# Optimization experiments

Measured on AMD Instinct MI355X. Metric: run time of the kernel, lower is better.

Reference implementation:

```python
import jax, jax.numpy as jnp
import numpy as np

H = 4096        # hidden_size
NH = 32         # num_attention_heads
NKV = 8         # num_key_value_heads
HD = H // NH    # head_dim = 128
N_REP = NH // NKV
SCALE = HD ** -0.5


def _rope(x, cos, sin):
    # x: (B, h, S, HD); cos/sin: (S, HD//2) broadcast over batch/heads
    x1 = x[..., 0::2]
    x2 = x[..., 1::2]
    return jnp.concatenate([x1 * cos - x2 * sin, x1 * sin + x2 * cos], axis=-1)


def setup_inputs() -> dict:
    key = jax.random.key(0)
    ks = jax.random.split(key, 9)
    B, S = 2, 2048
    return {
        "hidden_states": jax.random.normal(ks[0], (B, S, H), jnp.float32),
        "cos": jax.random.uniform(ks[1], (S, HD // 2), jnp.float32),
        "sin": jax.random.uniform(ks[2], (S, HD // 2), jnp.float32),
        "Wq": jax.random.normal(ks[3], (H, H), jnp.float32) * (H ** -0.5),
        "Wk": jax.random.normal(ks[4], (NKV * HD, H), jnp.float32) * (H ** -0.5),
        "bk": jax.random.normal(ks[5], (NKV * HD,), jnp.float32) * 0.01,
        "Wv": jax.random.normal(ks[6], (NKV * HD, H), jnp.float32) * (H ** -0.5),
        "bv": jax.random.normal(ks[7], (NKV * HD,), jnp.float32) * 0.01,
        "Wo": jax.random.normal(ks[8], (H, H), jnp.float32) * (H ** -0.5),
    }


def reference(hidden_states, cos, sin, Wq, Wk, bk, Wv, bv, Wo):
    B, S, _ = hidden_states.shape
    # projections (torch Linear: x @ W.T + b)
    q = (hidden_states @ Wq.T).reshape(B, S, NH, HD).transpose(0, 2, 1, 3)
    k = (hidden_states @ Wk.T + bk).reshape(B, S, NKV, HD).transpose(0, 2, 1, 3)
    v = (hidden_states @ Wv.T + bv).reshape(B, S, NKV, HD).transpose(0, 2, 1, 3)
    q = _rope(q, cos, sin)
    k = _rope(k, cos, sin)
    # GQA repeat_kv: (B, NKV, S, HD) -> (B, NH, S, HD)
    k = jnp.repeat(k, N_REP, axis=1)
    v = jnp.repeat(v, N_REP, axis=1)
    # full attention (no mask is actually applied in the source forward)
    scores = jnp.einsum('bhqd,bhkd->bhqk', q, k) * SCALE
    attn = jax.nn.softmax(scores, axis=-1)
    out = jnp.einsum('bhqk,bhkd->bhqd', attn, v)
    out = out.transpose(0, 2, 1, 3).reshape(B, S, H)
    return out @ Wo.T
```

## Files before the change

kernel.cpp:

```cpp
#include <hip/hip_runtime.h>

typedef unsigned short u16;
typedef short short8 __attribute__((ext_vector_type(8)));
typedef float floatx4 __attribute__((ext_vector_type(4)));

#define H_ 4096
#define NH_ 32
#define NKV_ 8
#define HD_ 128
#define SEQ_ 2048
#define BATCH_ 2
#define ROWS_ (BATCH_*SEQ_)
#define KVW_ (NKV_*HD_)
#define NQKV_ (H_ + 2*KVW_)
#define VSTRIDE_ NQKV_
#define SCALE_ 0.08838834764831845f
#define TSCALE_ (SCALE_*1.442695040888963f)

__device__ __forceinline__ u16 f2bf(float f) {
  union { float f; unsigned u; } x; x.f = f;
  unsigned r = x.u + 0x7fffu + ((x.u >> 16) & 1u);
  return (u16)(r >> 16);
}
__device__ __forceinline__ float bf2f(u16 h) {
  union { unsigned u; float f; } x; x.u = ((unsigned)h) << 16;
  return x.f;
}
__device__ __forceinline__ unsigned cvt_pk_bf16(float lo, float hi) {
  unsigned r;
  asm("v_cvt_pk_bf16_f32 %0, %1, %2" : "=v"(r) : "v"(lo), "v"(hi));
  return r;
}

__global__ __launch_bounds__(256) void cvt_f32_bf16(const float* __restrict__ src,
                                                    u16* __restrict__ dst, int n4) {
  int i = blockIdx.x * 256 + threadIdx.x;
  if (i >= n4) return;
  float4 v = ((const float4*)src)[i];
  ushort4 o;
  o.x = f2bf(v.x); o.y = f2bf(v.y); o.z = f2bf(v.z); o.w = f2bf(v.w);
  ((ushort4*)dst)[i] = o;
}

__global__ __launch_bounds__(256) void bias_concat(const float* __restrict__ bk,
                                                   const float* __restrict__ bv,
                                                   float* __restrict__ dst) {
  int i = blockIdx.x * 256 + threadIdx.x;
  if (i >= NQKV_) return;
  float v = 0.f;
  if (i >= H_ + KVW_)      v = bv[i - (H_ + KVW_)];
  else if (i >= H_)        v = bk[i - H_];
  dst[i] = v;
}

template<int BF16_OUT, int HAS_BIAS>
__global__ __launch_bounds__(512, 2) void gemm_nt_8p(const u16* __restrict__ A, const u16* __restrict__ B,
                                                     const float* __restrict__ bias, void* __restrict__ Cout,
                                                     int M, int N, int K)
{
  __shared__ __align__(16) u16 lds[65536];
  char* ldsB = (char*)lds;
  const int tid  = threadIdx.x;
  const int lane = tid & 63;
  const int wave = tid >> 6;
  const int ln   = lane & 15;
  const int quad = lane >> 4;
  const int wm   = wave >> 2;
  const int wn   = wave & 3;

  const int NB  = N >> 8;
  const int nwg = gridDim.x;
  const int cpx = nwg >> 3;
  const int l   = (blockIdx.x & 7) * cpx + (blockIdx.x >> 3);
  const int m0  = (l / NB) * 256;
  const int n0  = (l % NB) * 256;

  const u16* srcp[4][2];
  {
    int ob0 = wave*2048 + lane*16;
#pragma unroll
    for (int h = 0; h < 4; ++h) {
#pragma unroll
      for (int j = 0; j < 2; ++j) {
        int ob  = ob0 + j*1024;
        int row = ob >> 6;
        int sl  = ((ob >> 4) & 3) ^ ((row >> 1) & 3);
        int kst = h >> 1;
        if ((h & 1) == 0) srcp[h][j] = A + (size_t)(m0 + row)*K + kst*32 + sl*8;
        else              srcp[h][j] = B + (size_t)(n0 + row)*K + kst*32 + sl*8;
      }
    }
  }

#define STAGE(h_, p_, kt_)                                                          \
  {                                                                                 \
    __builtin_amdgcn_global_load_lds(                                               \
      (const __attribute__((address_space(1))) void*)(srcp[h_][0] + (kt_)*64),      \
      (__attribute__((address_space(3))) void*)(ldsB + (((h_)&1)*65536 + (p_)*32768 \
          + ((h_)>>1)*16384 + wave*2048)), 16, 0, 0);                               \
    __builtin_amdgcn_global_load_lds(                                               \
      (const __attribute__((address_space(1))) void*)(srcp[h_][1] + (kt_)*64),      \
      (__attribute__((address_space(3))) void*)(ldsB + (((h_)&1)*65536 + (p_)*32768 \
          + ((h_)>>1)*16384 + wave*2048 + 1024)), 16, 0, 0);                        \
  }

  const int slq16 = (quad ^ ((ln >> 1) & 3)) * 16;
  const int aoffL = (wm*128 + ln)*64 + slq16;
  const int boffL = (wn*64  + ln)*64 + slq16;

  floatx4 zf = {0.f, 0.f, 0.f, 0.f};
  floatx4 acc[8][4];
#pragma unroll
  for (int i = 0; i < 8; ++i)
#pragma unroll
    for (int j = 0; j < 4; ++j) acc[i][j] = zf;

  STAGE(0, 0, 0) STAGE(1, 0, 0) STAGE(2, 0, 0) STAGE(3, 0, 0)
  asm volatile("s_waitcnt vmcnt(4)");
  __builtin_amdgcn_s_barrier();

  const int NT = K >> 6;
  for (int t = 0; t < NT; ++t) {
    const int p  = t & 1;
    const int np = p ^ 1;
    const char* ab = ldsB + p*32768;
    const char* bb = ldsB + 65536 + p*32768;
    short8 af[4], bq[4];

#pragma unroll
    for (int j = 0; j < 4; ++j) bq[j] = *(const short8*)(bb + boffL + j*1024);
#pragma unroll
    for (int i = 0; i < 4; ++i) af[i] = *(const short8*)(ab + aoffL + i*1024);
    if (t + 1 < NT) STAGE(0, np, t+1)
    __builtin_amdgcn_s_barrier();
    asm volatile("s_waitcnt lgkmcnt(0)");
    __builtin_amdgcn_sched_barrier(0);
    __builtin_amdgcn_s_setprio(1);
#pragma unroll
    for (int i = 0; i < 4; ++i)
#pragma unroll
      for (int j = 0; j < 4; ++j)
        acc[i][j] = __builtin_amdgcn_mfma_f32_16x16x32_bf16(af[i], bq[j], acc[i][j], 0, 0, 0);
    __builtin_amdgcn_s_setprio(0);
    __builtin_amdgcn_s_barrier();

#pragma unroll
    for (int i = 0; i < 4; ++i) af[i] = *(const short8*)(ab + aoffL + (4+i)*1024);
    if (t + 1 < NT) STAGE(1, np, t+1)
    __builtin_amdgcn_s_barrier();
    asm volatile("s_waitcnt lgkmcnt(0)");
    __builtin_amdgcn_sched_barrier(0);
    __builtin_amdgcn_s_setprio(1);
#pragma unroll
    for (int i = 0; i < 4; ++i)
#pragma unroll
      for (int j = 0; j < 4; ++j)
        acc[4+i][j] = __builtin_amdgcn_mfma_f32_16x16x32_bf16(af[i], bq[j], acc[4+i][j], 0, 0, 0);
    __builtin_amdgcn_s_setprio(0);
    if (t + 1 < NT) { asm volatile("s_waitcnt vmcnt(4)"); }
    else            { asm volatile("s_waitcnt vmcnt(0)"); }
    __builtin_amdgcn_s_barrier();

#pragma unroll
    for (int j = 0; j < 4; ++j) bq[j] = *(const short8*)(bb + 16384 + boffL + j*1024);
#pragma unroll
    for (int i = 0; i < 4; ++i) af[i] = *(const short8*)(ab + 16384 + aoffL + i*1024);
    if (t + 1 < NT) STAGE(2, np, t+1)
    __builtin_amdgcn_s_barrier();
    asm volatile("s_waitcnt lgkmcnt(0)");
    __builtin_amdgcn_sched_barrier(0);
    __builtin_amdgcn_s_setprio(1);
#pragma unroll
    for (int i = 0; i < 4; ++i)
#pragma unroll
      for (int j = 0; j < 4; ++j)
        acc[i][j] = __builtin_amdgcn_mfma_f32_16x16x32_bf16(af[i], bq[j], acc[i][j], 0, 0, 0);
    __builtin_amdgcn_s_setprio(0);
    __builtin_amdgcn_s_barrier();

#pragma unroll
    for (int i = 0; i < 4; ++i) af[i] = *(const short8*)(ab + 16384 + aoffL + (4+i)*1024);
    if (t + 1 < NT) STAGE(3, np, t+1)
    __builtin_amdgcn_s_barrier();
    asm volatile("s_waitcnt lgkmcnt(0)");
    __builtin_amdgcn_sched_barrier(0);
    __builtin_amdgcn_s_setprio(1);
#pragma unroll
    for (int i = 0; i < 4; ++i)
#pragma unroll
      for (int j = 0; j < 4; ++j)
        acc[4+i][j] = __builtin_amdgcn_mfma_f32_16x16x32_bf16(af[i], bq[j], acc[4+i][j], 0, 0, 0);
    __builtin_amdgcn_s_setprio(0);
    if (t + 1 < NT) { asm volatile("s_waitcnt vmcnt(4)"); }
    __builtin_amdgcn_s_barrier();
  }
#undef STAGE

#pragma unroll
  for (int i = 0; i < 8; ++i) {
#pragma unroll
    for (int j = 0; j < 4; ++j) {
      int row = m0 + wm*128 + i*16 + quad*4;
      int col = n0 + wn*64  + j*16 + ln;
      float bv_ = HAS_BIAS ? bias[col] : 0.f;
#pragma unroll
      for (int r = 0; r < 4; ++r) {
        float v = acc[i][j][r] + bv_;
        if (BF16_OUT) ((u16*)Cout)[(size_t)(row+r)*N + col] = f2bf(v);
        else          ((float*)Cout)[(size_t)(row+r)*N + col] = v;
      }
    }
  }
}

template<int BF16_OUT, int HAS_BIAS>
__global__ __launch_bounds__(512, 2) void gemm_nt_8p_h(const u16* __restrict__ A, const u16* __restrict__ B,
                                                       const float* __restrict__ bias, void* __restrict__ Cout,
                                                       int M, int N, int K)
{
  __shared__ __align__(16) u16 lds[49152];
  char* ldsB = (char*)lds;
  const int tid  = threadIdx.x;
  const int lane = tid & 63;
  const int wave = tid >> 6;
  const int ln   = lane & 15;
  const int quad = lane >> 4;
  const int wm   = wave >> 2;
  const int wn   = wave & 3;

  const int NB  = N >> 8;
  const int nwg = gridDim.x;
  const int cpx = nwg >> 3;
  const int l   = (blockIdx.x & 7) * cpx + (blockIdx.x >> 3);
  const int m0  = (l / NB) * 128;
  const int n0  = (l % NB) * 256;

  const u16* srcA[2];
  const u16* srcB[2][2];
  {
    int ob  = wave*1024 + lane*16;
    int row = ob >> 6;
    int sl  = ((ob >> 4) & 3) ^ ((row >> 1) & 3);
#pragma unroll
    for (int kst = 0; kst < 2; ++kst)
      srcA[kst] = A + (size_t)(m0 + row)*K + kst*32 + sl*8;
  }
#pragma unroll
  for (int j = 0; j < 2; ++j) {
    int ob  = wave*2048 + j*1024 + lane*16;
    int row = ob >> 6;
    int sl  = ((ob >> 4) & 3) ^ ((row >> 1) & 3);
#pragma unroll
    for (int kst = 0; kst < 2; ++kst)
      srcB[kst][j] = B + (size_t)(n0 + row)*K + kst*32 + sl*8;
  }

#define STAGEH(kst_, p_, kt_)                                                        \
  {                                                                                  \
    __builtin_amdgcn_global_load_lds(                                                \
      (const __attribute__((address_space(1))) void*)(srcA[kst_] + (kt_)*64),        \
      (__attribute__((address_space(3))) void*)(ldsB + ((p_)*16384 + (kst_)*8192     \
          + wave*1024)), 16, 0, 0);                                                  \
    __builtin_amdgcn_global_load_lds(                                                \
      (const __attribute__((address_space(1))) void*)(srcB[kst_][0] + (kt_)*64),     \
      (__attribute__((address_space(3))) void*)(ldsB + (32768 + (p_)*32768           \
          + (kst_)*16384 + wave*2048)), 16, 0, 0);                                   \
    __builtin_amdgcn_global_load_lds(                                                \
      (const __attribute__((address_space(1))) void*)(srcB[kst_][1] + (kt_)*64),     \
      (__attribute__((address_space(3))) void*)(ldsB + (32768 + (p_)*32768           \
          + (kst_)*16384 + wave*2048 + 1024)), 16, 0, 0);                            \
  }

  const int slq16 = (quad ^ ((ln >> 1) & 3)) * 16;
  const int aoffL = (wm*64 + ln)*64 + slq16;
  const int boffL = (wn*64 + ln)*64 + slq16;

  floatx4 zf = {0.f, 0.f, 0.f, 0.f};
  floatx4 acc[4][4];
#pragma unroll
  for (int i = 0; i < 4; ++i)
#pragma unroll
    for (int j = 0; j < 4; ++j) acc[i][j] = zf;

  STAGEH(0, 0, 0) STAGEH(1, 0, 0)
  asm volatile("s_waitcnt vmcnt(3)");
  __builtin_amdgcn_s_barrier();

  const int NT = K >> 6;
  for (int t = 0; t < NT; ++t) {
    const int p  = t & 1;
    const int np = p ^ 1;
    const char* ab = ldsB + p*16384;
    const char* bb = ldsB + 32768 + p*32768;
    short8 af[4], bq[4];

#pragma unroll
    for (int j = 0; j < 4; ++j) bq[j] = *(const short8*)(bb + boffL + j*1024);
#pragma unroll
    for (int i = 0; i < 4; ++i) af[i] = *(const short8*)(ab + aoffL + i*1024);
    if (t + 1 < NT) STAGEH(0, np, t+1)
    __builtin_amdgcn_s_barrier();
    asm volatile("s_waitcnt lgkmcnt(0)");
    __builtin_amdgcn_sched_barrier(0);
    __builtin_amdgcn_s_setprio(1);
#pragma unroll
    for (int i = 0; i < 4; ++i)
#pragma unroll
      for (int j = 0; j < 4; ++j)
        acc[i][j] = __builtin_amdgcn_mfma_f32_16x16x32_bf16(af[i], bq[j], acc[i][j], 0, 0, 0);
    __builtin_amdgcn_s_setprio(0);
    if (t + 1 < NT) { asm volatile("s_waitcnt vmcnt(3)"); }
    else            { asm volatile("s_waitcnt vmcnt(0)"); }
    __builtin_amdgcn_s_barrier();

#pragma unroll
    for (int j = 0; j < 4; ++j) bq[j] = *(const short8*)(bb + 16384 + boffL + j*1024);
#pragma unroll
    for (int i = 0; i < 4; ++i) af[i] = *(const short8*)(ab + 8192 + aoffL + i*1024);
    if (t + 1 < NT) STAGEH(1, np, t+1)
    __builtin_amdgcn_s_barrier();
    asm volatile("s_waitcnt lgkmcnt(0)");
    __builtin_amdgcn_sched_barrier(0);
    __builtin_amdgcn_s_setprio(1);
#pragma unroll
    for (int i = 0; i < 4; ++i)
#pragma unroll
      for (int j = 0; j < 4; ++j)
        acc[i][j] = __builtin_amdgcn_mfma_f32_16x16x32_bf16(af[i], bq[j], acc[i][j], 0, 0, 0);
    __builtin_amdgcn_s_setprio(0);
    if (t + 1 < NT) { asm volatile("s_waitcnt vmcnt(3)"); }
    __builtin_amdgcn_s_barrier();
  }
#undef STAGEH

#pragma unroll
  for (int i = 0; i < 4; ++i) {
#pragma unroll
    for (int j = 0; j < 4; ++j) {
      int row = m0 + wm*64 + i*16 + quad*4;
      int col = n0 + wn*64 + j*16 + ln;
      float bv_ = HAS_BIAS ? bias[col] : 0.f;
#pragma unroll
      for (int r = 0; r < 4; ++r) {
        float v = acc[i][j][r] + bv_;
        if (BF16_OUT) ((u16*)Cout)[(size_t)(row+r)*N + col] = f2bf(v);
        else          ((float*)Cout)[(size_t)(row+r)*N + col] = v;
      }
    }
  }
}

__global__ __launch_bounds__(256) void rope_kernel(const u16* __restrict__ X, u16* __restrict__ Y,
                                                   const float* __restrict__ cosb, const float* __restrict__ sinb,
                                                   int nheads, int total, int istride, int ostride)
{
  int idx = blockIdx.x * 256 + threadIdx.x;
  if (idx >= total) return;
  int d = idx & 63;
  int t = idx >> 6;
  int hh = t % nheads;
  int row = t / nheads;
  int s = row & (SEQ_ - 1);
  size_t bi = (size_t)row * istride + hh * HD_;
  size_t bo = (size_t)row * ostride + hh * HD_;
  float x1 = bf2f(X[bi + 2*d]);
  float x2 = bf2f(X[bi + 2*d + 1]);
  float c  = cosb[s*64 + d];
  float sn = sinb[s*64 + d];
  Y[bo + d]      = f2bf(x1*c - x2*sn);
  Y[bo + 64 + d] = f2bf(x1*sn + x2*c);
}

#define KS_TILE (64*128)

__global__ __launch_bounds__(512, 2) void attn_fwd(const u16* __restrict__ Q, const u16* __restrict__ K,
                                                   const u16* __restrict__ V, u16* __restrict__ O)
{
  __shared__ __align__(16) u16 Ks[2*KS_TILE];
  __shared__ __align__(16) u16 Vt[128*72];
  const int tid  = threadIdx.x;
  const int lane = tid & 63;
  const int wave = tid >> 6;
  const int ln   = lane & 15;
  const int quad = lane >> 4;
  const int lin = (blockIdx.x & 7) * 64 + (blockIdx.x >> 3);
  const int bh  = lin >> 3;
  const int b   = bh >> 5;
  const int h   = bh & 31;
  const int kvh = h >> 2;
  const int q0  = (lin & 7) * 256;

  short8 qf[2][4];
#pragma unroll
  for (int mt = 0; mt < 2; ++mt) {
    const u16* qbase = Q + (size_t)(b*SEQ_ + q0 + wave*32 + mt*16 + ln) * H_ + h * HD_;
#pragma unroll
    for (int kst = 0; kst < 4; ++kst)
      qf[mt][kst] = *(const short8*)(qbase + kst*32 + quad*8);
  }

  short8 bones;
  {
    short v1 = (ln == 0) ? (short)0x3F80 : (short)0;
#pragma unroll
    for (int j = 0; j < 8; ++j) bones[j] = v1;
  }

  int kou[2];
  const u16* ks0[2];
#pragma unroll
  for (int i = 0; i < 2; ++i) {
    int ou = wave*2048 + i*1024;
    int ob = ou + lane*16;
    int key = ob >> 8;
    int dgp = (ob >> 4) & 15;
    int dgl = dgp ^ (key & 15);
    kou[i] = ou;
    ks0[i] = K + (size_t)(b*SEQ_ + key)*KVW_ + kvh*HD_ + dgl*8;
  }
  const int g  = tid & 15;
  const int dg = (tid >> 4) & 15;
  const int j2 = tid >> 8;
  const u16* vs0 = V + (size_t)(b*SEQ_ + j2*32 + g)*VSTRIDE_ + kvh*HD_ + dg*8;
  const int k0v = ((g >> 1) & 1)*32 + (g >> 2)*8 + (g & 1)*4 + j2*2;

  floatx4 zf = {0.f, 0.f, 0.f, 0.f};
  floatx4 o[2][8];
  floatx4 ol[2];
#pragma unroll
  for (int mt = 0; mt < 2; ++mt) {
    ol[mt] = zf;
#pragma unroll
    for (int jt = 0; jt < 8; ++jt) o[mt][jt] = zf;
  }
  float mrow[2] = {-1e30f, -1e30f};

  int4 vreg[2];
#pragma unroll
  for (int i = 0; i < 2; ++i)
    __builtin_amdgcn_global_load_lds((const __attribute__((address_space(1))) void*)ks0[i],
        (__attribute__((address_space(3))) void*)((char*)Ks + kou[i]), 16, 0, 0);
#pragma unroll
  for (int jj = 0; jj < 2; ++jj)
    vreg[jj] = *(const int4*)(vs0 + (size_t)(jj*16)*VSTRIDE_);
  {
    union { int4 v; u16 u[8]; } w[2];
    w[0].v = vreg[0]; w[1].v = vreg[1];
#pragma unroll
    for (int dd = 0; dd < 8; ++dd) {
      ushort2 t2; t2.x = w[0].u[dd]; t2.y = w[1].u[dd];
      *(ushort2*)&Vt[(dg*8 + dd)*72 + k0v] = t2;
    }
  }
  __syncthreads();

  const int NT = SEQ_ / 64;
  for (int t = 0; t < NT; ++t) {
    if (t + 1 < NT) {
      size_t roff = (size_t)(t+1) * 64 * KVW_;
      char* kb = (char*)Ks + ((t+1)&1) * (KS_TILE*2);
#pragma unroll
      for (int i = 0; i < 2; ++i)
        __builtin_amdgcn_global_load_lds((const __attribute__((address_space(1))) void*)(ks0[i] + roff),
            (__attribute__((address_space(3))) void*)(kb + kou[i]), 16, 0, 0);
      size_t voff = (size_t)(t+1) * 64 * VSTRIDE_;
#pragma unroll
      for (int jj = 0; jj < 2; ++jj)
        vreg[jj] = *(const int4*)(vs0 + voff + (size_t)(jj*16)*VSTRIDE_);
    }
    const u16* Kc = Ks + (t&1)*KS_TILE;

    floatx4 s[2][4];
#pragma unroll
    for (int nt = 0; nt < 4; ++nt) { s[0][nt] = zf; s[1][nt] = zf; }
    __builtin_amdgcn_s_setprio(1);
#pragma unroll
    for (int kst = 0; kst < 4; ++kst) {
      int dgp = (kst*4 + quad) ^ ln;
#pragma unroll
      for (int nt = 0; nt < 4; ++nt) {
        short8 kf = *(const short8*)&Kc[(nt*16 + ln)*128 + dgp*8];
        s[0][nt] = __builtin_amdgcn_mfma_f32_16x16x32_bf16(kf, qf[0][kst], s[0][nt], 0, 0, 0);
        s[1][nt] = __builtin_amdgcn_mfma_f32_16x16x32_bf16(kf, qf[1][kst], s[1][nt], 0, 0, 0);
      }
    }
    __builtin_amdgcn_s_setprio(0);

    float rmv[2];
    bool ok = true;
#pragma unroll
    for (int mt = 0; mt < 2; ++mt) {
      float m0_ = fmaxf(fmaxf(s[mt][0][0], s[mt][0][1]), fmaxf(s[mt][0][2], s[mt][0][3]));
      float m1_ = fmaxf(fmaxf(s[mt][1][0], s[mt][1][1]), fmaxf(s[mt][1][2], s[mt][1][3]));
      float m2_ = fmaxf(fmaxf(s[mt][2][0], s[mt][2][1]), fmaxf(s[mt][2][2], s[mt][2][3]));
      float m3_ = fmaxf(fmaxf(s[mt][3][0], s[mt][3][1]), fmaxf(s[mt][3][2], s[mt][3][3]));
      float rm = fmaxf(fmaxf(m0_, m1_), fmaxf(m2_, m3_)) * TSCALE_;
      rm = fmaxf(rm, __shfl_xor(rm, 16));
      rm = fmaxf(rm, __shfl_xor(rm, 32));
      rmv[mt] = rm;
      ok = ok && (rm - mrow[mt] <= 8.0f);
    }
    if (!__all(ok)) {
#pragma unroll
      for (int mt = 0; mt < 2; ++mt) {
        float mn = fmaxf(mrow[mt], rmv[mt]);
        float al = exp2f(mrow[mt] - mn);
        mrow[mt] = mn;
        float av[4];
#pragma unroll
        for (int r = 0; r < 4; ++r) av[r] = __shfl(al, (lane & 48) | (quad*4 + r));
#pragma unroll
        for (int r = 0; r < 4; ++r) {
          float a_ = av[r];
#pragma unroll
          for (int jt = 0; jt < 8; ++jt) o[mt][jt][r] *= a_;
          ol[mt][r] *= a_;
        }
      }
    }
    short8 pa[2][2];
#pragma unroll
    for (int mt = 0; mt < 2; ++mt) {
      float mn = mrow[mt];
      float p[4][4];
#pragma unroll
      for (int nt = 0; nt < 4; ++nt)
#pragma unroll
        for (int r = 0; r < 4; ++r)
          p[r][nt] = exp2f(fmaf(s[mt][nt][r], TSCALE_, -mn));
#pragma unroll
      for (int k2 = 0; k2 < 2; ++k2) {
        union { unsigned u[4]; short8 v; } pk;
        pk.u[0] = cvt_pk_bf16(p[2*k2][0],   p[2*k2][1]);
        pk.u[1] = cvt_pk_bf16(p[2*k2][2],   p[2*k2][3]);
        pk.u[2] = cvt_pk_bf16(p[2*k2+1][0], p[2*k2+1][1]);
        pk.u[3] = cvt_pk_bf16(p[2*k2+1][2], p[2*k2+1][3]);
        pa[mt][k2] = pk.v;
      }
    }

    __builtin_amdgcn_s_setprio(1);
#pragma unroll
    for (int k2 = 0; k2 < 2; ++k2) {
#pragma unroll
      for (int jt = 0; jt < 8; ++jt) {
        short8 vf = *(const short8*)&Vt[(jt*16 + ln)*72 + k2*32 + quad*8];
        o[0][jt] = __builtin_amdgcn_mfma_f32_16x16x32_bf16(pa[0][k2], vf, o[0][jt], 0, 0, 0);
        o[1][jt] = __builtin_amdgcn_mfma_f32_16x16x32_bf16(pa[1][k2], vf, o[1][jt], 0, 0, 0);
      }
      ol[0] = __builtin_amdgcn_mfma_f32_16x16x32_bf16(pa[0][k2], bones, ol[0], 0, 0, 0);
      ol[1] = __builtin_amdgcn_mfma_f32_16x16x32_bf16(pa[1][k2], bones, ol[1], 0, 0, 0);
    }
    __builtin_amdgcn_s_setprio(0);

    __syncthreads();
    if (t + 1 < NT) {
      union { int4 v; u16 u[8]; } w[2];
      w[0].v = vreg[0]; w[1].v = vreg[1];
#pragma unroll
      for (int dd = 0; dd < 8; ++dd) {
        ushort2 t2; t2.x = w[0].u[dd]; t2.y = w[1].u[dd];
        *(ushort2*)&Vt[(dg*8 + dd)*72 + k0v] = t2;
      }
    }
    __syncthreads();
  }

#pragma unroll
  for (int mt = 0; mt < 2; ++mt) {
#pragma unroll
    for (int r = 0; r < 4; ++r) {
      float lv = __shfl(ol[mt][r], lane & 48);
      float inv = 1.f / lv;
      size_t row = (size_t)(b*SEQ_ + q0 + wave*32 + mt*16 + quad*4 + r);
      u16* dst = O + row * H_ + h * HD_ + ln;
#pragma unroll
      for (int jt = 0; jt < 8; ++jt)
        dst[jt*16] = f2bf(o[mt][jt][r] * inv);
    }
  }
}

extern "C" void kernel_launch(void* const* d_in, const int* in_sizes, int n_in,
                              void* d_out, int out_size, void* d_ws, size_t ws_size,
                              hipStream_t stream) {
  const float* hs   = (const float*)d_in[0];
  const float* cosb = (const float*)d_in[1];
  const float* sinb = (const float*)d_in[2];
  const float* Wq   = (const float*)d_in[3];
  const float* Wk   = (const float*)d_in[4];
  const float* bk   = (const float*)d_in[5];
  const float* Wv   = (const float*)d_in[6];
  const float* bv   = (const float*)d_in[7];
  const float* Wo   = (const float*)d_in[8];
  float* out = (float*)d_out;

  char* ws = (char*)d_ws;
  u16*   hs_bf   = (u16*)(ws +          0);
  u16*   Wqkv_bf = (u16*)(ws +   33554432);
  u16*   Wo_bf   = (u16*)(ws +   83886080);
  u16*   QKV0    = (u16*)(ws +  117440512);
  u16*   Qr      = (u16*)(ws +  167772160);
  u16*   Kr      = (u16*)(ws +  201326592);
  float* biasqkv = (float*)(ws + 209715200);
  u16*   Oa      = hs_bf;

  {
    int n;
    n = ROWS_*H_;  cvt_f32_bf16<<<(n/4 + 255)/256, 256, 0, stream>>>(hs, hs_bf, n/4);
    n = H_*H_;     cvt_f32_bf16<<<(n/4 + 255)/256, 256, 0, stream>>>(Wq, Wqkv_bf, n/4);
    n = KVW_*H_;   cvt_f32_bf16<<<(n/4 + 255)/256, 256, 0, stream>>>(Wk, Wqkv_bf + (size_t)H_*H_, n/4);
    n = KVW_*H_;   cvt_f32_bf16<<<(n/4 + 255)/256, 256, 0, stream>>>(Wv, Wqkv_bf + (size_t)(H_+KVW_)*H_, n/4);
    n = H_*H_;     cvt_f32_bf16<<<(n/4 + 255)/256, 256, 0, stream>>>(Wo, Wo_bf, n/4);
    bias_concat<<<(NQKV_ + 255)/256, 256, 0, stream>>>(bk, bv, biasqkv);
  }

  gemm_nt_8p_h<1,1><<<dim3((ROWS_/128)*(NQKV_/256)), dim3(512), 0, stream>>>(hs_bf, Wqkv_bf, biasqkv, QKV0, ROWS_, NQKV_, H_);
  rope_kernel<<<(ROWS_*NH_*64)/256,  256, 0, stream>>>(QKV0,       Qr, cosb, sinb, NH_,  ROWS_*NH_*64,  NQKV_, H_);
  rope_kernel<<<(ROWS_*NKV_*64)/256, 256, 0, stream>>>(QKV0 + H_,  Kr, cosb, sinb, NKV_, ROWS_*NKV_*64, NQKV_, KVW_);
  attn_fwd<<<dim3(512), dim3(512), 0, stream>>>(Qr, Kr, QKV0 + H_ + KVW_, Oa);
  gemm_nt_8p<0,0><<<dim3((ROWS_/256)*(H_/256)), dim3(512), 0, stream>>>(Oa, Wo_bf, nullptr, out, ROWS_, H_, H_);
}
```

Baseline: 822.3 us.

## Fuse fp32-to-bf16 conversions into one grid-stride kernel and remap GEMM tiles per XCD

Replaces five separate fp32-to-bf16 conversion launches with a single grid-stride kernel that dispatches on a flat index, removing launch overhead and tail effects. Both GEMM kernels get a new block-to-tile mapping that gives each XCD a compact 2D patch of output tiles (8x4 or 8x4 per round), so the A and B panels a chiplet reads are reused in its local L2. The mappings hardcode the grid dimensions for these problem sizes, and the grid-stride loop with per-element branching adds some index overhead.

```diff
diff --git a/kernel.cpp b/kernel.cpp
--- a/kernel.cpp
+++ b/kernel.cpp
@@ -32,14 +32,26 @@
   return r;
 }
 
-__global__ __launch_bounds__(256) void cvt_f32_bf16(const float* __restrict__ src,
-                                                    u16* __restrict__ dst, int n4) {
-  int i = blockIdx.x * 256 + threadIdx.x;
-  if (i >= n4) return;
-  float4 v = ((const float4*)src)[i];
-  ushort4 o;
-  o.x = f2bf(v.x); o.y = f2bf(v.y); o.z = f2bf(v.z); o.w = f2bf(v.w);
-  ((ushort4*)dst)[i] = o;
+__global__ __launch_bounds__(256) void cvt_all(const float* __restrict__ hs, const float* __restrict__ Wq,
+                                               const float* __restrict__ Wk, const float* __restrict__ Wv,
+                                               const float* __restrict__ Wo,
+                                               u16* __restrict__ hs_bf, u16* __restrict__ Wqkv_bf,
+                                               u16* __restrict__ Wo_bf) {
+  const int n_hs = ROWS_*H_/4;
+  const int n_wq = H_*H_/4;
+  const int n_wk = KVW_*H_/4;
+  const long total = (long)n_hs + n_wq + 2*(long)n_wk + n_wq;
+  for (long i = (long)blockIdx.x*256 + threadIdx.x; i < total; i += (long)gridDim.x*256) {
+    const float* s; u16* d; long j = i;
+    if (j < n_hs)                       { s = hs; d = hs_bf; }
+    else if ((j -= n_hs) < n_wq)        { s = Wq; d = Wqkv_bf; }
+    else if ((j -= n_wq) < n_wk)        { s = Wk; d = Wqkv_bf + (size_t)H_*H_; }
+    else if ((j -= n_wk) < n_wk)        { s = Wv; d = Wqkv_bf + (size_t)(H_+KVW_)*H_; }
+    else { j -= n_wk;                     s = Wo; d = Wo_bf; }
+    float4 v = ((const float4*)s)[j];
+    ushort4 o; o.x = f2bf(v.x); o.y = f2bf(v.y); o.z = f2bf(v.z); o.w = f2bf(v.w);
+    ((ushort4*)d)[j] = o;
+  }
 }
 
 __global__ __launch_bounds__(256) void bias_concat(const float* __restrict__ bk,
@@ -68,12 +80,10 @@
   const int wm   = wave >> 2;
   const int wn   = wave & 3;
 
-  const int NB  = N >> 8;
-  const int nwg = gridDim.x;
-  const int cpx = nwg >> 3;
-  const int l   = (blockIdx.x & 7) * cpx + (blockIdx.x >> 3);
-  const int m0  = (l / NB) * 256;
-  const int n0  = (l % NB) * 256;
+  const int xcd = blockIdx.x & 7;
+  const int k_  = blockIdx.x >> 3;
+  const int m0  = ((xcd >> 2) * 8 + (k_ & 7)) * 256;
+  const int n0  = ((xcd & 3) * 4 + (k_ >> 3)) * 256;
 
   const u16* srcp[4][2];
   {
@@ -228,12 +238,12 @@
   const int wm   = wave >> 2;
   const int wn   = wave & 3;
 
-  const int NB  = N >> 8;
-  const int nwg = gridDim.x;
-  const int cpx = nwg >> 3;
-  const int l   = (blockIdx.x & 7) * cpx + (blockIdx.x >> 3);
-  const int m0  = (l / NB) * 128;
-  const int n0  = (l % NB) * 256;
+  const int xcd = blockIdx.x & 7;
+  const int w_  = blockIdx.x >> 3;
+  const int rnd = w_ >> 5;
+  const int wi  = w_ & 31;
+  const int m0  = ((xcd >> 1) * 8 + (wi & 7)) * 128;
+  const int n0  = (rnd * 8 + (xcd & 1) * 4 + (wi >> 3)) * 256;
 
   const u16* srcA[2];
   const u16* srcB[2][2];
@@ -605,15 +615,8 @@
   float* biasqkv = (float*)(ws + 209715200);
   u16*   Oa      = hs_bf;
 
-  {
-    int n;
-    n = ROWS_*H_;  cvt_f32_bf16<<<(n/4 + 255)/256, 256, 0, stream>>>(hs, hs_bf, n/4);
-    n = H_*H_;     cvt_f32_bf16<<<(n/4 + 255)/256, 256, 0, stream>>>(Wq, Wqkv_bf, n/4);
-    n = KVW_*H_;   cvt_f32_bf16<<<(n/4 + 255)/256, 256, 0, stream>>>(Wk, Wqkv_bf + (size_t)H_*H_, n/4);
-    n = KVW_*H_;   cvt_f32_bf16<<<(n/4 + 255)/256, 256, 0, stream>>>(Wv, Wqkv_bf + (size_t)(H_+KVW_)*H_, n/4);
-    n = H_*H_;     cvt_f32_bf16<<<(n/4 + 255)/256, 256, 0, stream>>>(Wo, Wo_bf, n/4);
-    bias_concat<<<(NQKV_ + 255)/256, 256, 0, stream>>>(bk, bv, biasqkv);
-  }
+  cvt_all<<<2048, 256, 0, stream>>>(hs, Wq, Wk, Wv, Wo, hs_bf, Wqkv_bf, Wo_bf);
+  bias_concat<<<(NQKV_ + 255)/256, 256, 0, stream>>>(bk, bv, biasqkv);
 
   gemm_nt_8p_h<1,1><<<dim3((ROWS_/128)*(NQKV_/256)), dim3(512), 0, stream>>>(hs_bf, Wqkv_bf, biasqkv, QKV0, ROWS_, NQKV_, H_);
   rope_kernel<<<(ROWS_*NH_*64)/256,  256, 0, stream>>>(QKV0,       Qr, cosb, sinb, NH_,  ROWS_*NH_*64,  NQKV_, H_);
```

After: 785.7 us. -4.4%, faster.
